# Kernel optimization log

Measured on AMD Instinct MI355X. Metric: run time of the kernel, lower is better.

## Reference

```python
import jax, jax.numpy as jnp
import numpy as np

B, S, HID = 4, 2048, 512
NH, HD = 8, 64
MAX_REL = 512


def setup_inputs() -> dict:
    key = jax.random.key(0)
    ks = jax.random.split(key, 10)
    sd = 0.02
    return {
        "hidden_states": jax.random.normal(ks[0], (B, S, HID), jnp.float32),
        "attention_mask": jnp.ones((B, S), jnp.float32),
        "Wq": jax.random.normal(ks[1], (HID, HID), jnp.float32) * sd,
        "bq": jnp.zeros((HID,), jnp.float32),
        "Wk": jax.random.normal(ks[2], (HID, HID), jnp.float32) * sd,
        "bk": jnp.zeros((HID,), jnp.float32),
        "Wv": jax.random.normal(ks[3], (HID, HID), jnp.float32) * sd,
        "bv": jnp.zeros((HID,), jnp.float32),
        "Wo": jax.random.normal(ks[4], (HID, HID), jnp.float32) * sd,
        "bo": jnp.zeros((HID,), jnp.float32),
        "rel_table": jax.random.normal(ks[5], (2 * MAX_REL + 1, NH), jnp.float32) * sd,
    }


def _heads(x):
    # [B,S,HID] -> [B,NH,S,HD]
    return x.reshape(B, S, NH, HD).transpose(0, 2, 1, 3)


def reference(hidden_states, attention_mask, Wq, bq, Wk, bk, Wv, bv, Wo, bo, rel_table):
    q = _heads(hidden_states @ Wq + bq)
    k = _heads(hidden_states @ Wk + bk)
    v = _heads(hidden_states @ Wv + bv)

    scores = jnp.einsum("bhqd,bhkd->bhqk", q, k) / jnp.sqrt(jnp.float32(HD))

    # relative position bias: rel[i,j] = clip(j-i, -MAX_REL, MAX_REL) + MAX_REL
    pos = jnp.arange(S)
    rel = jnp.clip(pos[None, :] - pos[:, None], -MAX_REL, MAX_REL) + MAX_REL
    bias = rel_table[rel]                      # [S,S,NH]
    bias = bias.transpose(2, 0, 1)             # [NH,S,S]
    scores = scores + bias[None]

    # mask: 1 attend, 0 masked
    neg = jnp.finfo(scores.dtype).min
    scores = scores + (1.0 - attention_mask)[:, None, None, :] * neg

    probs = jax.nn.softmax(scores, axis=-1)
    ctx = jnp.einsum("bhqk,bhkd->bhqd", probs, v)
    ctx = ctx.transpose(0, 2, 1, 3).reshape(B, S, HID)
    return ctx @ Wo + bo
```

## Files before the change

### kernel.cpp

```cpp
#include <hip/hip_runtime.h>
#include <hip/hip_bf16.h>

#define B_    4
#define S_    2048
#define HID_  512
#define NH_   8
#define HD_   64
#define MAXREL 512
#define M_    (B_ * S_)

#define LOG2E 1.44269504f
#define SCALE_Q (0.125f * LOG2E)

typedef __attribute__((ext_vector_type(8))) short bf8;
typedef __attribute__((ext_vector_type(4))) float f4;

static __device__ __forceinline__ unsigned short f2bf(float f) {
    union { float f; unsigned int u; } v; v.f = f;
    unsigned int u = v.u;
    unsigned int r = (u + 0x7FFFu + ((u >> 16) & 1u)) >> 16;
    return (unsigned short)r;
}

static __device__ __forceinline__ float ex2(float x) {
    float r; asm("v_exp_f32 %0, %1" : "=v"(r) : "v"(x)); return r;
}

static __device__ __forceinline__ void gload16(const void* g, void* l) {
    __builtin_amdgcn_global_load_lds(
        (const __attribute__((address_space(1))) unsigned int*)g,
        (__attribute__((address_space(3))) unsigned int*)l, 16, 0, 0);
}

#define MFMA16(a, b, c) __builtin_amdgcn_mfma_f32_16x16x32_bf16((a), (b), (c), 0, 0, 0)

__global__ void k_cast_hs(const float* __restrict__ src, unsigned short* __restrict__ dst, int n4) {
    int i = blockIdx.x * blockDim.x + threadIdx.x;
    if (i >= n4) return;
    float4 v = ((const float4*)src)[i];
    ushort4 o;
    o.x = f2bf(v.x); o.y = f2bf(v.y); o.z = f2bf(v.z); o.w = f2bf(v.w);
    ((ushort4*)dst)[i] = o;
}

__global__ void k_prep_mask(const float* __restrict__ mask, float* __restrict__ maskadd) {
    int i = blockIdx.x * blockDim.x + threadIdx.x;
    if (i < M_) maskadd[i] = (1.0f - mask[i]) * -3.0e38f;
}

__global__ void k_transpose_w4(const float* __restrict__ W0, const float* __restrict__ W1,
                               const float* __restrict__ W2, const float* __restrict__ W3,
                               unsigned short* __restrict__ T0, unsigned short* __restrict__ T1,
                               unsigned short* __restrict__ T2, unsigned short* __restrict__ T3) {
    __shared__ float tile[32][33];
    const int z = blockIdx.z;
    const float* W = (z == 0) ? W0 : (z == 1) ? W1 : (z == 2) ? W2 : W3;
    unsigned short* T = (z == 0) ? T0 : (z == 1) ? T1 : (z == 2) ? T2 : T3;
    const int tx = threadIdx.x & 31, ty = threadIdx.x >> 5;
    const int n0 = blockIdx.x * 32, k0 = blockIdx.y * 32;
    #pragma unroll
    for (int i = 0; i < 4; ++i)
        tile[ty + i * 8][tx] = W[(size_t)(k0 + ty + i * 8) * HID_ + n0 + tx];
    __syncthreads();
    #pragma unroll
    for (int i = 0; i < 4; ++i)
        T[(size_t)(n0 + ty + i * 8) * HID_ + k0 + tx] = f2bf(tile[tx][ty + i * 8]);
}

__global__ __launch_bounds__(256, 3) void k_gemm_qkv(
    const unsigned short* __restrict__ Abf,
    const unsigned short* __restrict__ Wqt, const unsigned short* __restrict__ Wkt,
    const unsigned short* __restrict__ Wvt,
    const float* __restrict__ bq, const float* __restrict__ bk, const float* __restrict__ bv,
    unsigned short* __restrict__ Q, unsigned short* __restrict__ K, unsigned short* __restrict__ Vt)
{
    __shared__ unsigned short Al[2][128 * 32];
    __shared__ unsigned short Bl[2][128 * 32];

    const int t = threadIdx.x;
    const int lane = t & 63, w = t >> 6;
    const int lr = lane & 15, lg = lane >> 4;
    const int wr = w >> 1, wc = w & 1;

    const int m0 = blockIdx.x * 128;
    const int ng = blockIdx.y * 128;
    const int z = ng >> 9;
    const int n0 = ng & 511;
    const unsigned short* Wt = (z == 0) ? Wqt : ((z == 1) ? Wkt : Wvt);
    const float* bias = (z == 0) ? bq : ((z == 1) ? bk : bv);
    const float osc = (z == 0) ? SCALE_Q : 1.0f;

    const int srow = t >> 2;
    const int sc = (((t & 3) ^ ((srow >> 1) & 3))) * 8;
    const unsigned short* Ag0 = &Abf[(size_t)(m0 + srow) * HID_ + sc];
    const unsigned short* Ag1 = &Abf[(size_t)(m0 + 64 + srow) * HID_ + sc];
    const unsigned short* Bg0 = &Wt[(size_t)(n0 + srow) * HID_ + sc];
    const unsigned short* Bg1 = &Wt[(size_t)(n0 + 64 + srow) * HID_ + sc];
    char* dA0 = (char*)&Al[0][0] + w * 1024;
    char* dB0 = (char*)&Bl[0][0] + w * 1024;

    const int fx = (lr >> 1) & 3;
    int aoff[4], boff[4];
    #pragma unroll
    for (int i = 0; i < 4; ++i) {
        aoff[i] = (wr * 64 + i * 16 + lr) * 32 + ((lg ^ fx) * 8);
        boff[i] = (wc * 64 + i * 16 + lr) * 32 + ((lg ^ fx) * 8);
    }

    gload16(Ag0, dA0);
    gload16(Ag1, dA0 + 4096);
    gload16(Bg0, dB0);
    gload16(Bg1, dB0 + 4096);
    __syncthreads();

    f4 acc[4][4] = {};
    for (int kt = 0; kt < 16; ++kt) {
        const int cur = kt & 1;
        if (kt < 15) {
            const int ko = (kt + 1) * 32;
            const int bo = (cur ^ 1) * 8192;
            gload16(Ag0 + ko, dA0 + bo);
            gload16(Ag1 + ko, dA0 + bo + 4096);
            gload16(Bg0 + ko, dB0 + bo);
            gload16(Bg1 + ko, dB0 + bo + 4096);
        }
        bf8 af[4], bf_[4];
        #pragma unroll
        for (int i = 0; i < 4; ++i) {
            af[i]  = *(const bf8*)&Al[cur][aoff[i]];
            bf_[i] = *(const bf8*)&Bl[cur][boff[i]];
        }
        #pragma unroll
        for (int mi = 0; mi < 4; ++mi)
            #pragma unroll
            for (int ni = 0; ni < 4; ++ni)
                acc[mi][ni] = MFMA16(af[mi], bf_[ni], acc[mi][ni]);
        __syncthreads();
    }

    #pragma unroll
    for (int mi = 0; mi < 4; ++mi)
    #pragma unroll
    for (int ni = 0; ni < 4; ++ni) {
        const int col = n0 + wc * 64 + ni * 16 + lr;
        const int h = col >> 6, d = col & 63;
        const float bs = bias[col];
        const int row0 = m0 + wr * 64 + mi * 16 + lg * 4;
        const int b = row0 >> 11, s0 = row0 & 2047;
        if (z == 2) {
            ushort4 o;
            o.x = f2bf(acc[mi][ni][0] + bs);
            o.y = f2bf(acc[mi][ni][1] + bs);
            o.z = f2bf(acc[mi][ni][2] + bs);
            o.w = f2bf(acc[mi][ni][3] + bs);
            *(ushort4*)&Vt[(((size_t)(b * NH_ + h)) * HD_ + d) * S_ + s0] = o;
        } else {
            unsigned short* dst = (z == 0) ? Q : K;
            #pragma unroll
            for (int r = 0; r < 4; ++r) {
                float v = (acc[mi][ni][r] + bs) * osc;
                dst[(((size_t)(b * NH_ + h)) * S_ + s0 + r) * HD_ + d] = f2bf(v);
            }
        }
    }
}

__global__ __launch_bounds__(512) void k_gemm_out(
    const unsigned short* __restrict__ Abf,
    const unsigned short* __restrict__ Wot,
    const float* __restrict__ bo,
    float* __restrict__ out)
{
    __shared__ unsigned short Al[2][128 * 32];
    __shared__ unsigned short Bl[2][128 * 32];

    const int t = threadIdx.x;
    const int lane = t & 63, w = t >> 6;
    const int lr = lane & 15, lg = lane >> 4;
    const int wr = w >> 2, wc = w & 3;

    const int m0 = blockIdx.x * 128;
    const int n0 = blockIdx.y * 128;

    const int srow = t >> 2;
    const int sc = (((t & 3) ^ ((srow >> 1) & 3))) * 8;
    const unsigned short* Ag = &Abf[(size_t)(m0 + srow) * HID_ + sc];
    const unsigned short* Bg = &Wot[(size_t)(n0 + srow) * HID_ + sc];
    char* dA = (char*)&Al[0][0] + w * 1024;
    char* dB = (char*)&Bl[0][0] + w * 1024;

    const int fx = (lr >> 1) & 3;
    int aoff[4], boff[2];
    #pragma unroll
    for (int i = 0; i < 4; ++i)
        aoff[i] = (wr * 64 + i * 16 + lr) * 32 + ((lg ^ fx) * 8);
    #pragma unroll
    for (int i = 0; i < 2; ++i)
        boff[i] = (wc * 32 + i * 16 + lr) * 32 + ((lg ^ fx) * 8);

    gload16(Ag, dA);
    gload16(Bg, dB);
    __syncthreads();

    f4 acc[4][2] = {};
    for (int kt = 0; kt < 16; ++kt) {
        const int cur = kt & 1;
        if (kt < 15) {
            const int ko = (kt + 1) * 32;
            const int bo_ = (cur ^ 1) * 8192;
            gload16(Ag + ko, dA + bo_);
            gload16(Bg + ko, dB + bo_);
        }
        bf8 af[4], bf_[2];
        #pragma unroll
        for (int i = 0; i < 4; ++i) af[i] = *(const bf8*)&Al[cur][aoff[i]];
        #pragma unroll
        for (int i = 0; i < 2; ++i) bf_[i] = *(const bf8*)&Bl[cur][boff[i]];
        #pragma unroll
        for (int mi = 0; mi < 4; ++mi)
            #pragma unroll
            for (int ni = 0; ni < 2; ++ni)
                acc[mi][ni] = MFMA16(af[mi], bf_[ni], acc[mi][ni]);
        __syncthreads();
    }

    #pragma unroll
    for (int mi = 0; mi < 4; ++mi)
    #pragma unroll
    for (int ni = 0; ni < 2; ++ni) {
        const int col = n0 + wc * 32 + ni * 16 + lr;
        const float bs = bo[col];
        const int row0 = m0 + wr * 64 + mi * 16 + lg * 4;
        #pragma unroll
        for (int r = 0; r < 4; ++r)
            out[(size_t)(row0 + r) * HID_ + col] = acc[mi][ni][r] + bs;
    }
}

__global__ __launch_bounds__(512, 4) void k_flash(
    const unsigned short* __restrict__ Q, const unsigned short* __restrict__ K,
    const unsigned short* __restrict__ Vt,
    const float* __restrict__ rel_table, const float* __restrict__ maskadd,
    unsigned short* __restrict__ ctx)
{
    __shared__ unsigned short Klds[2][4096];
    __shared__ unsigned short Vlds[2][4096];
    __shared__ unsigned short Ps[8][16][72];
    __shared__ float Tbp[2176];

    const int t = threadIdx.x;
    const int lane = t & 63, w = t >> 6;
    const int lr = lane & 15, lg = lane >> 4;

    const int flat = blockIdx.x;
    const int idx = flat >> 3;
    const int bh = (flat & 7) * 4 + (idx >> 4);
    const int qb = idx & 15;
    const int b = bh >> 3, h = bh & 7;
    const int q0 = qb * 128;

    for (int i = t; i < 2176; i += 512) {
        int r = i - q0 - 127;
        r = r < -MAXREL ? -MAXREL : (r > MAXREL ? MAXREL : r);
        Tbp[i] = rel_table[(r + MAXREL) * NH_ + h] * LOG2E;
    }
    const float TbLo = rel_table[h] * LOG2E;
    const float TbHi = rel_table[2 * MAXREL * NH_ + h] * LOG2E;

    const unsigned short* Kb = K + (size_t)bh * S_ * HD_;
    const unsigned short* Vb = Vt + (size_t)bh * HD_ * S_;
    const float* mb = maskadd + b * S_;

    const int myq = q0 + w * 16 + lr;
    const int qw = q0 + w * 16;
    bf8 qf0, qf1;
    {
        const unsigned short* qg = &Q[((size_t)bh * S_ + myq) * HD_ + lg * 8];
        qf0 = *(const bf8*)qg;
        qf1 = *(const bf8*)(qg + 32);
    }

    const int srow = w * 8 + (lane >> 3);
    const int scol = ((lane & 7) ^ (srow & 7)) * 8;
    const size_t kbase = (size_t)srow * HD_ + scol;
    const size_t vbase = (size_t)srow * S_ + scol;
    const int woff = w * 1024;

    f4 cacc[4] = {};
    float m_s = -INFINITY, lsum = 0.f;

    gload16(&Kb[kbase], (char*)&Klds[0][0] + woff);
    gload16(&Vb[vbase], (char*)&Vlds[0][0] + woff);
    __syncthreads();

    const int xr = lr & 7;
    const int jb0 = 127 - w * 16 - lr + lg * 4;
    for (int ti = 0; ti < 32; ++ti) {
        const int cur = ti & 1;
        const int kv0 = ti * 64;

        if (ti < 31) {
            const int nxt = cur ^ 1;
            gload16(&Kb[kbase + (size_t)(kv0 + 64) * HD_], (char*)&Klds[nxt][0] + woff);
            gload16(&Vb[vbase + kv0 + 64], (char*)&Vlds[nxt][0] + woff);
        }

        float4 mk[4];
        #pragma unroll
        for (int nt = 0; nt < 4; ++nt)
            mk[nt] = *(const float4*)&mb[kv0 + nt * 16 + lg * 4];

        f4 sa[4];
        #pragma unroll
        for (int nt = 0; nt < 4; ++nt) {
            const int row = (nt * 16 + lr) * 64;
            bf8 kf0 = *(const bf8*)&Klds[cur][row + ((0 + lg) ^ xr) * 8];
            bf8 kf1 = *(const bf8*)&Klds[cur][row + ((4 + lg) ^ xr) * 8];
            f4 u = {};
            u = MFMA16(kf0, qf0, u);
            u = MFMA16(kf1, qf1, u);
            sa[nt] = u;
        }

        float tmaxl = -INFINITY;
        const bool uniLo = (kv0 + 63 - qw <= -MAXREL);
        const bool uniHi = (kv0 - qw - 15 >= MAXREL);
        if (uniLo || uniHi) {
            const float biasC = uniLo ? TbLo : TbHi;
            #pragma unroll
            for (int nt = 0; nt < 4; ++nt) {
                #pragma unroll
                for (int r = 0; r < 4; ++r) {
                    float mkv = (r == 0) ? mk[nt].x : (r == 1) ? mk[nt].y : (r == 2) ? mk[nt].z : mk[nt].w;
                    float sv = sa[nt][r] + (biasC + mkv);
                    sa[nt][r] = sv;
                    tmaxl = fmaxf(tmaxl, sv);
                }
            }
        } else {
            const int jb = jb0 + kv0;
            #pragma unroll
            for (int nt = 0; nt < 4; ++nt) {
                #pragma unroll
                for (int r = 0; r < 4; ++r) {
                    float mkv = (r == 0) ? mk[nt].x : (r == 1) ? mk[nt].y : (r == 2) ? mk[nt].z : mk[nt].w;
                    float sv = sa[nt][r] + (Tbp[jb + nt * 16 + r] + mkv);
                    sa[nt][r] = sv;
                    tmaxl = fmaxf(tmaxl, sv);
                }
            }
        }
        float tmax = fmaxf(tmaxl, __shfl_xor(tmaxl, 16));
        tmax = fmaxf(tmax, __shfl_xor(tmax, 32));

        float ptile = 0.f;
        unsigned int pk[8];
        #pragma unroll
        for (int nt = 0; nt < 4; ++nt) {
            float p0 = ex2(sa[nt][0] - m_s);
            float p1 = ex2(sa[nt][1] - m_s);
            float p2 = ex2(sa[nt][2] - m_s);
            float p3 = ex2(sa[nt][3] - m_s);
            ptile += (p0 + p1) + (p2 + p3);
            asm("v_cvt_pk_bf16_f32 %0, %1, %2" : "=v"(pk[nt * 2])     : "v"(p0), "v"(p1));
            asm("v_cvt_pk_bf16_f32 %0, %1, %2" : "=v"(pk[nt * 2 + 1]) : "v"(p2), "v"(p3));
        }
        if (!__all(tmax <= m_s + 8.0f)) {
            const float mnew = fmaxf(m_s, tmax);
            const float fac = ex2(m_s - mnew);
            lsum *= fac;
            #pragma unroll
            for (int dt = 0; dt < 4; ++dt)
                #pragma unroll
                for (int r = 0; r < 4; ++r) cacc[dt][r] *= fac;
            ptile = 0.f;
            #pragma unroll
            for (int nt = 0; nt < 4; ++nt) {
                float p0 = ex2(sa[nt][0] - mnew);
                float p1 = ex2(sa[nt][1] - mnew);
                float p2 = ex2(sa[nt][2] - mnew);
                float p3 = ex2(sa[nt][3] - mnew);
                ptile += (p0 + p1) + (p2 + p3);
                asm("v_cvt_pk_bf16_f32 %0, %1, %2" : "=v"(pk[nt * 2])     : "v"(p0), "v"(p1));
                asm("v_cvt_pk_bf16_f32 %0, %1, %2" : "=v"(pk[nt * 2 + 1]) : "v"(p2), "v"(p3));
            }
            m_s = mnew;
        }
        lsum += ptile;

        #pragma unroll
        for (int nt = 0; nt < 4; ++nt) {
            uint2 pv; pv.x = pk[nt * 2]; pv.y = pk[nt * 2 + 1];
            *(uint2*)&Ps[w][lr][nt * 16 + lg * 4] = pv;
        }
        asm volatile("s_waitcnt lgkmcnt(0)" ::: "memory");
        __builtin_amdgcn_sched_barrier(0);

        #pragma unroll
        for (int kc = 0; kc < 2; ++kc) {
            bf8 pb = *(const bf8*)&Ps[w][lr][kc * 32 + lg * 8];
            #pragma unroll
            for (int dt = 0; dt < 4; ++dt) {
                const int row = (dt * 16 + lr) * 64;
                bf8 vf = *(const bf8*)&Vlds[cur][row + ((kc * 4 + lg) ^ xr) * 8];
                cacc[dt] = MFMA16(vf, pb, cacc[dt]);
            }
        }
        __syncthreads();
    }

    lsum += __shfl_xor(lsum, 16);
    lsum += __shfl_xor(lsum, 32);
    const float inv = 1.0f / lsum;
    unsigned short* cg = &ctx[(size_t)(b * S_ + myq) * HID_ + h * HD_];
    #pragma unroll
    for (int dt = 0; dt < 4; ++dt) {
        ushort4 o;
        o.x = f2bf(cacc[dt][0] * inv);
        o.y = f2bf(cacc[dt][1] * inv);
        o.z = f2bf(cacc[dt][2] * inv);
        o.w = f2bf(cacc[dt][3] * inv);
        *(ushort4*)&cg[dt * 16 + lg * 4] = o;
    }
}

extern "C" void kernel_launch(void* const* d_in, const int* in_sizes, int n_in,
                              void* d_out, int out_size, void* d_ws, size_t ws_size,
                              hipStream_t stream) {
    const float* hs  = (const float*)d_in[0];
    const float* msk = (const float*)d_in[1];
    const float* Wq  = (const float*)d_in[2];
    const float* bq  = (const float*)d_in[3];
    const float* Wk  = (const float*)d_in[4];
    const float* bk  = (const float*)d_in[5];
    const float* Wv  = (const float*)d_in[6];
    const float* bv  = (const float*)d_in[7];
    const float* Wo  = (const float*)d_in[8];
    const float* bo  = (const float*)d_in[9];
    const float* rel = (const float*)d_in[10];
    float* out = (float*)d_out;

    char* ws = (char*)d_ws;
    unsigned short* hsb = (unsigned short*)ws; ws += (size_t)M_ * HID_ * 2;
    unsigned short* Wqt = (unsigned short*)ws; ws += (size_t)HID_ * HID_ * 2;
    unsigned short* Wkt = (unsigned short*)ws; ws += (size_t)HID_ * HID_ * 2;
    unsigned short* Wvt = (unsigned short*)ws; ws += (size_t)HID_ * HID_ * 2;
    unsigned short* Wot = (unsigned short*)ws; ws += (size_t)HID_ * HID_ * 2;
    unsigned short* Qb  = (unsigned short*)ws; ws += (size_t)M_ * HID_ * 2;
    unsigned short* Kb  = (unsigned short*)ws; ws += (size_t)M_ * HID_ * 2;
    unsigned short* Vtb = (unsigned short*)ws; ws += (size_t)M_ * HID_ * 2;
    unsigned short* ctxb= (unsigned short*)ws; ws += (size_t)M_ * HID_ * 2;
    float* maskadd      = (float*)ws;          ws += (size_t)M_ * 4;

    k_cast_hs<<<(M_ * HID_ / 4 + 255) / 256, 256, 0, stream>>>(hs, hsb, M_ * HID_ / 4);
    k_prep_mask<<<(M_ + 255) / 256, 256, 0, stream>>>(msk, maskadd);
    k_transpose_w4<<<dim3(16, 16, 4), 256, 0, stream>>>(Wq, Wk, Wv, Wo, Wqt, Wkt, Wvt, Wot);
    k_gemm_qkv<<<dim3(64, 12), 256, 0, stream>>>(
        hsb, Wqt, Wkt, Wvt, bq, bk, bv, Qb, Kb, Vtb);
    k_flash<<<512, 512, 0, stream>>>(Qb, Kb, Vtb, rel, maskadd, ctxb);
    k_gemm_out<<<dim3(64, 4), 512, 0, stream>>>(ctxb, Wot, bo, out);
}
```

Baseline: 115.7 us.

## Switch flash attention to 32x32 MFMA with 4 waves of 32 query rows

The attention kernel moves from 16x16x32 to 32x32x16 bf16 MFMA tiles. The block drops from 8 waves of 16 queries to 4 waves of 32 queries, so each K/V fragment read from LDS feeds more compute, and each thread now issues two async loads per tile instead of one. It also raises wave priority around the MFMA sections and reduces the cross-lane max/sum shuffles to a single xor step. The cost is more accumulator registers per wave and fewer waves per block, which may lower latency hiding.

```diff
diff --git a/kernel.cpp b/kernel.cpp
--- a/kernel.cpp
+++ b/kernel.cpp
@@ -14,6 +14,7 @@
 
 typedef __attribute__((ext_vector_type(8))) short bf8;
 typedef __attribute__((ext_vector_type(4))) float f4;
+typedef __attribute__((ext_vector_type(16))) float f16f;
 
 static __device__ __forceinline__ unsigned short f2bf(float f) {
     union { float f; unsigned int u; } v; v.f = f;
@@ -33,6 +34,7 @@
 }
 
 #define MFMA16(a, b, c) __builtin_amdgcn_mfma_f32_16x16x32_bf16((a), (b), (c), 0, 0, 0)
+#define MFMA32(a, b, c) __builtin_amdgcn_mfma_f32_32x32x16_bf16((a), (b), (c), 0, 0, 0)
 
 __global__ void k_cast_hs(const float* __restrict__ src, unsigned short* __restrict__ dst, int n4) {
     int i = blockIdx.x * blockDim.x + threadIdx.x;
@@ -237,7 +239,7 @@
     }
 }
 
-__global__ __launch_bounds__(512, 4) void k_flash(
+__global__ __launch_bounds__(256, 2) void k_flash(
     const unsigned short* __restrict__ Q, const unsigned short* __restrict__ K,
     const unsigned short* __restrict__ Vt,
     const float* __restrict__ rel_table, const float* __restrict__ maskadd,
@@ -245,12 +247,12 @@
 {
     __shared__ unsigned short Klds[2][4096];
     __shared__ unsigned short Vlds[2][4096];
-    __shared__ unsigned short Ps[8][16][72];
+    __shared__ unsigned short Ps[4][32][68];
     __shared__ float Tbp[2176];
 
     const int t = threadIdx.x;
     const int lane = t & 63, w = t >> 6;
-    const int lr = lane & 15, lg = lane >> 4;
+    const int q = lane & 31, hi = lane >> 5;
 
     const int flat = blockIdx.x;
     const int idx = flat >> 3;
@@ -259,7 +261,7 @@
     const int b = bh >> 3, h = bh & 7;
     const int q0 = qb * 128;
 
-    for (int i = t; i < 2176; i += 512) {
+    for (int i = t; i < 2176; i += 256) {
         int r = i - q0 - 127;
         r = r < -MAXREL ? -MAXREL : (r > MAXREL ? MAXREL : r);
         Tbp[i] = rel_table[(r + MAXREL) * NH_ + h] * LOG2E;
@@ -271,156 +273,197 @@
     const unsigned short* Vb = Vt + (size_t)bh * HD_ * S_;
     const float* mb = maskadd + b * S_;
 
-    const int myq = q0 + w * 16 + lr;
-    const int qw = q0 + w * 16;
-    bf8 qf0, qf1;
-    {
-        const unsigned short* qg = &Q[((size_t)bh * S_ + myq) * HD_ + lg * 8];
-        qf0 = *(const bf8*)qg;
-        qf1 = *(const bf8*)(qg + 32);
-    }
-
-    const int srow = w * 8 + (lane >> 3);
-    const int scol = ((lane & 7) ^ (srow & 7)) * 8;
-    const size_t kbase = (size_t)srow * HD_ + scol;
-    const size_t vbase = (size_t)srow * S_ + scol;
+    const int myq = q0 + w * 32 + q;
+    const int qw = q0 + w * 32;
+    bf8 qf[4];
+    #pragma unroll
+    for (int s = 0; s < 4; ++s)
+        qf[s] = *(const bf8*)&Q[((size_t)bh * S_ + myq) * HD_ + s * 16 + hi * 8];
+
+    const int srow = t >> 3, sslot = t & 7;
+    const int sxor = (sslot ^ (srow & 7)) * 8;
+    const size_t kb0 = (size_t)srow * HD_ + sxor;
+    const size_t kb1 = (size_t)(srow + 32) * HD_ + sxor;
+    const size_t vb0 = (size_t)srow * S_ + sxor;
+    const size_t vb1 = (size_t)(srow + 32) * S_ + sxor;
     const int woff = w * 1024;
 
-    f4 cacc[4] = {};
+    f16f ca0 = {}, ca1 = {};
     float m_s = -INFINITY, lsum = 0.f;
 
-    gload16(&Kb[kbase], (char*)&Klds[0][0] + woff);
-    gload16(&Vb[vbase], (char*)&Vlds[0][0] + woff);
+    gload16(&Kb[kb0], (char*)&Klds[0][0] + woff);
+    gload16(&Kb[kb1], (char*)&Klds[0][0] + 4096 + woff);
+    gload16(&Vb[vb0], (char*)&Vlds[0][0] + woff);
+    gload16(&Vb[vb1], (char*)&Vlds[0][0] + 4096 + woff);
     __syncthreads();
 
-    const int xr = lr & 7;
-    const int jb0 = 127 - w * 16 - lr + lg * 4;
+    const int xq = q & 7;
+    const int jb0 = 127 - w * 32 - q + 4 * hi;
     for (int ti = 0; ti < 32; ++ti) {
         const int cur = ti & 1;
         const int kv0 = ti * 64;
 
         if (ti < 31) {
             const int nxt = cur ^ 1;
-            gload16(&Kb[kbase + (size_t)(kv0 + 64) * HD_], (char*)&Klds[nxt][0] + woff);
-            gload16(&Vb[vbase + kv0 + 64], (char*)&Vlds[nxt][0] + woff);
-        }
-
-        float4 mk[4];
-        #pragma unroll
-        for (int nt = 0; nt < 4; ++nt)
-            mk[nt] = *(const float4*)&mb[kv0 + nt * 16 + lg * 4];
-
-        f4 sa[4];
-        #pragma unroll
-        for (int nt = 0; nt < 4; ++nt) {
-            const int row = (nt * 16 + lr) * 64;
-            bf8 kf0 = *(const bf8*)&Klds[cur][row + ((0 + lg) ^ xr) * 8];
-            bf8 kf1 = *(const bf8*)&Klds[cur][row + ((4 + lg) ^ xr) * 8];
-            f4 u = {};
-            u = MFMA16(kf0, qf0, u);
-            u = MFMA16(kf1, qf1, u);
-            sa[nt] = u;
-        }
+            const size_t ko = (size_t)(kv0 + 64) * HD_;
+            gload16(&Kb[kb0 + ko], (char*)&Klds[nxt][0] + woff);
+            gload16(&Kb[kb1 + ko], (char*)&Klds[nxt][0] + 4096 + woff);
+            gload16(&Vb[vb0 + kv0 + 64], (char*)&Vlds[nxt][0] + woff);
+            gload16(&Vb[vb1 + kv0 + 64], (char*)&Vlds[nxt][0] + 4096 + woff);
+        }
+
+        f16f sa0 = {}, sa1 = {};
+        __builtin_amdgcn_s_setprio(1);
+        #pragma unroll
+        for (int s = 0; s < 4; ++s) {
+            const int slot = ((2 * s + hi) ^ xq) * 8;
+            bf8 k0 = *(const bf8*)&Klds[cur][q * 64 + slot];
+            bf8 k1 = *(const bf8*)&Klds[cur][(q + 32) * 64 + slot];
+            sa0 = MFMA32(k0, qf[s], sa0);
+            sa1 = MFMA32(k1, qf[s], sa1);
+        }
+        __builtin_amdgcn_s_setprio(0);
 
         float tmaxl = -INFINITY;
-        const bool uniLo = (kv0 + 63 - qw <= -MAXREL);
-        const bool uniHi = (kv0 - qw - 15 >= MAXREL);
-        if (uniLo || uniHi) {
-            const float biasC = uniLo ? TbLo : TbHi;
-            #pragma unroll
-            for (int nt = 0; nt < 4; ++nt) {
+        {
+            const bool ulo = (kv0 + 31 - qw <= -MAXREL);
+            const bool uhi = (kv0 - (qw + 31) >= MAXREL);
+            if (ulo || uhi) {
+                const float bc = ulo ? TbLo : TbHi;
                 #pragma unroll
-                for (int r = 0; r < 4; ++r) {
-                    float mkv = (r == 0) ? mk[nt].x : (r == 1) ? mk[nt].y : (r == 2) ? mk[nt].z : mk[nt].w;
-                    float sv = sa[nt][r] + (biasC + mkv);
-                    sa[nt][r] = sv;
-                    tmaxl = fmaxf(tmaxl, sv);
+                for (int m = 0; m < 4; ++m) {
+                    float4 mk = *(const float4*)&mb[kv0 + m * 8 + hi * 4];
+                    #pragma unroll
+                    for (int r = 0; r < 4; ++r) {
+                        float mkv = (r == 0) ? mk.x : (r == 1) ? mk.y : (r == 2) ? mk.z : mk.w;
+                        float sv = sa0[4 * m + r] + bc + mkv;
+                        sa0[4 * m + r] = sv;
+                        tmaxl = fmaxf(tmaxl, sv);
+                    }
+                }
+            } else {
+                #pragma unroll
+                for (int m = 0; m < 4; ++m) {
+                    float4 mk = *(const float4*)&mb[kv0 + m * 8 + hi * 4];
+                    #pragma unroll
+                    for (int r = 0; r < 4; ++r) {
+                        float mkv = (r == 0) ? mk.x : (r == 1) ? mk.y : (r == 2) ? mk.z : mk.w;
+                        float sv = sa0[4 * m + r] + Tbp[jb0 + kv0 + m * 8 + r] + mkv;
+                        sa0[4 * m + r] = sv;
+                        tmaxl = fmaxf(tmaxl, sv);
+                    }
                 }
             }
-        } else {
-            const int jb = jb0 + kv0;
-            #pragma unroll
-            for (int nt = 0; nt < 4; ++nt) {
+            const int kvh = kv0 + 32;
+            const bool ulo1 = (kvh + 31 - qw <= -MAXREL);
+            const bool uhi1 = (kvh - (qw + 31) >= MAXREL);
+            if (ulo1 || uhi1) {
+                const float bc = ulo1 ? TbLo : TbHi;
                 #pragma unroll
-                for (int r = 0; r < 4; ++r) {
-                    float mkv = (r == 0) ? mk[nt].x : (r == 1) ? mk[nt].y : (r == 2) ? mk[nt].z : mk[nt].w;
-                    float sv = sa[nt][r] + (Tbp[jb + nt * 16 + r] + mkv);
-                    sa[nt][r] = sv;
-                    tmaxl = fmaxf(tmaxl, sv);
+                for (int m = 0; m < 4; ++m) {
+                    float4 mk = *(const float4*)&mb[kvh + m * 8 + hi * 4];
+                    #pragma unroll
+                    for (int r = 0; r < 4; ++r) {
+                        float mkv = (r == 0) ? mk.x : (r == 1) ? mk.y : (r == 2) ? mk.z : mk.w;
+                        float sv = sa1[4 * m + r] + bc + mkv;
+                        sa1[4 * m + r] = sv;
+                        tmaxl = fmaxf(tmaxl, sv);
+                    }
+                }
+            } else {
+                #pragma unroll
+                for (int m = 0; m < 4; ++m) {
+                    float4 mk = *(const float4*)&mb[kvh + m * 8 + hi * 4];
+                    #pragma unroll
+                    for (int r = 0; r < 4; ++r) {
+                        float mkv = (r == 0) ? mk.x : (r == 1) ? mk.y : (r == 2) ? mk.z : mk.w;
+                        float sv = sa1[4 * m + r] + Tbp[jb0 + kvh + m * 8 + r] + mkv;
+                        sa1[4 * m + r] = sv;
+                        tmaxl = fmaxf(tmaxl, sv);
+                    }
                 }
             }
         }
-        float tmax = fmaxf(tmaxl, __shfl_xor(tmaxl, 16));
-        tmax = fmaxf(tmax, __shfl_xor(tmax, 32));
+        const float tmax = fmaxf(tmaxl, __shfl_xor(tmaxl, 32));
 
         float ptile = 0.f;
-        unsigned int pk[8];
-        #pragma unroll
-        for (int nt = 0; nt < 4; ++nt) {
-            float p0 = ex2(sa[nt][0] - m_s);
-            float p1 = ex2(sa[nt][1] - m_s);
-            float p2 = ex2(sa[nt][2] - m_s);
-            float p3 = ex2(sa[nt][3] - m_s);
-            ptile += (p0 + p1) + (p2 + p3);
-            asm("v_cvt_pk_bf16_f32 %0, %1, %2" : "=v"(pk[nt * 2])     : "v"(p0), "v"(p1));
-            asm("v_cvt_pk_bf16_f32 %0, %1, %2" : "=v"(pk[nt * 2 + 1]) : "v"(p2), "v"(p3));
+        unsigned int pkA[8], pkB[8];
+        #pragma unroll
+        for (int m = 0; m < 4; ++m) {
+            float a0 = ex2(sa0[4 * m + 0] - m_s), a1 = ex2(sa0[4 * m + 1] - m_s);
+            float a2 = ex2(sa0[4 * m + 2] - m_s), a3 = ex2(sa0[4 * m + 3] - m_s);
+            float b0 = ex2(sa1[4 * m + 0] - m_s), b1 = ex2(sa1[4 * m + 1] - m_s);
+            float b2 = ex2(sa1[4 * m + 2] - m_s), b3 = ex2(sa1[4 * m + 3] - m_s);
+            ptile += ((a0 + a1) + (a2 + a3)) + ((b0 + b1) + (b2 + b3));
+            asm("v_cvt_pk_bf16_f32 %0, %1, %2" : "=v"(pkA[2 * m])     : "v"(a0), "v"(a1));
+            asm("v_cvt_pk_bf16_f32 %0, %1, %2" : "=v"(pkA[2 * m + 1]) : "v"(a2), "v"(a3));
+            asm("v_cvt_pk_bf16_f32 %0, %1, %2" : "=v"(pkB[2 * m])     : "v"(b0), "v"(b1));
+            asm("v_cvt_pk_bf16_f32 %0, %1, %2" : "=v"(pkB[2 * m + 1]) : "v"(b2), "v"(b3));
         }
         if (!__all(tmax <= m_s + 8.0f)) {
             const float mnew = fmaxf(m_s, tmax);
             const float fac = ex2(m_s - mnew);
             lsum *= fac;
-            #pragma unroll
-            for (int dt = 0; dt < 4; ++dt)
-                #pragma unroll
-                for (int r = 0; r < 4; ++r) cacc[dt][r] *= fac;
+            ca0 *= fac;
+            ca1 *= fac;
             ptile = 0.f;
             #pragma unroll
-            for (int nt = 0; nt < 4; ++nt) {
-                float p0 = ex2(sa[nt][0] - mnew);
-                float p1 = ex2(sa[nt][1] - mnew);
-                float p2 = ex2(sa[nt][2] - mnew);
-                float p3 = ex2(sa[nt][3] - mnew);
-                ptile += (p0 + p1) + (p2 + p3);
-                asm("v_cvt_pk_bf16_f32 %0, %1, %2" : "=v"(pk[nt * 2])     : "v"(p0), "v"(p1));
-                asm("v_cvt_pk_bf16_f32 %0, %1, %2" : "=v"(pk[nt * 2 + 1]) : "v"(p2), "v"(p3));
+            for (int m = 0; m < 4; ++m) {
+                float a0 = ex2(sa0[4 * m + 0] - mnew), a1 = ex2(sa0[4 * m + 1] - mnew);
+                float a2 = ex2(sa0[4 * m + 2] - mnew), a3 = ex2(sa0[4 * m + 3] - mnew);
+                float b0 = ex2(sa1[4 * m + 0] - mnew), b1 = ex2(sa1[4 * m + 1] - mnew);
+                float b2 = ex2(sa1[4 * m + 2] - mnew), b3 = ex2(sa1[4 * m + 3] - mnew);
+                ptile += ((a0 + a1) + (a2 + a3)) + ((b0 + b1) + (b2 + b3));
+                asm("v_cvt_pk_bf16_f32 %0, %1, %2" : "=v"(pkA[2 * m])     : "v"(a0), "v"(a1));
+                asm("v_cvt_pk_bf16_f32 %0, %1, %2" : "=v"(pkA[2 * m + 1]) : "v"(a2), "v"(a3));
+                asm("v_cvt_pk_bf16_f32 %0, %1, %2" : "=v"(pkB[2 * m])     : "v"(b0), "v"(b1));
+                asm("v_cvt_pk_bf16_f32 %0, %1, %2" : "=v"(pkB[2 * m + 1]) : "v"(b2), "v"(b3));
             }
             m_s = mnew;
         }
         lsum += ptile;
 
         #pragma unroll
-        for (int nt = 0; nt < 4; ++nt) {
-            uint2 pv; pv.x = pk[nt * 2]; pv.y = pk[nt * 2 + 1];
-            *(uint2*)&Ps[w][lr][nt * 16 + lg * 4] = pv;
+        for (int m = 0; m < 4; ++m) {
+            uint2 pa; pa.x = pkA[2 * m]; pa.y = pkA[2 * m + 1];
+            *(uint2*)&Ps[w][q][m * 8 + hi * 4] = pa;
+            uint2 pb; pb.x = pkB[2 * m]; pb.y = pkB[2 * m + 1];
+            *(uint2*)&Ps[w][q][32 + m * 8 + hi * 4] = pb;
         }
         asm volatile("s_waitcnt lgkmcnt(0)" ::: "memory");
         __builtin_amdgcn_sched_barrier(0);
 
-        #pragma unroll
-        for (int kc = 0; kc < 2; ++kc) {
-            bf8 pb = *(const bf8*)&Ps[w][lr][kc * 32 + lg * 8];
-            #pragma unroll
-            for (int dt = 0; dt < 4; ++dt) {
-                const int row = (dt * 16 + lr) * 64;
-                bf8 vf = *(const bf8*)&Vlds[cur][row + ((kc * 4 + lg) ^ xr) * 8];
-                cacc[dt] = MFMA16(vf, pb, cacc[dt]);
-            }
-        }
+        __builtin_amdgcn_s_setprio(1);
+        #pragma unroll
+        for (int s = 0; s < 4; ++s) {
+            bf8 pf = *(const bf8*)&Ps[w][q][s * 16 + hi * 8];
+            const int slot = ((2 * s + hi) ^ xq) * 8;
+            bf8 v0 = *(const bf8*)&Vlds[cur][q * 64 + slot];
+            bf8 v1 = *(const bf8*)&Vlds[cur][(q + 32) * 64 + slot];
+            ca0 = MFMA32(v0, pf, ca0);
+            ca1 = MFMA32(v1, pf, ca1);
+        }
+        __builtin_amdgcn_s_setprio(0);
         __syncthreads();
     }
 
-    lsum += __shfl_xor(lsum, 16);
     lsum += __shfl_xor(lsum, 32);
     const float inv = 1.0f / lsum;
     unsigned short* cg = &ctx[(size_t)(b * S_ + myq) * HID_ + h * HD_];
     #pragma unroll
-    for (int dt = 0; dt < 4; ++dt) {
-        ushort4 o;
-        o.x = f2bf(cacc[dt][0] * inv);
-        o.y = f2bf(cacc[dt][1] * inv);
-        o.z = f2bf(cacc[dt][2] * inv);
-        o.w = f2bf(cacc[dt][3] * inv);
-        *(ushort4*)&cg[dt * 16 + lg * 4] = o;
+    for (int m = 0; m < 4; ++m) {
+        ushort4 o0;
+        o0.x = f2bf(ca0[4 * m + 0] * inv);
+        o0.y = f2bf(ca0[4 * m + 1] * inv);
+        o0.z = f2bf(ca0[4 * m + 2] * inv);
+        o0.w = f2bf(ca0[4 * m + 3] * inv);
+        *(ushort4*)&cg[m * 8 + hi * 4] = o0;
+        ushort4 o1;
+        o1.x = f2bf(ca1[4 * m + 0] * inv);
+        o1.y = f2bf(ca1[4 * m + 1] * inv);
+        o1.z = f2bf(ca1[4 * m + 2] * inv);
+        o1.w = f2bf(ca1[4 * m + 3] * inv);
+        *(ushort4*)&cg[32 + m * 8 + hi * 4] = o1;
     }
 }
 
@@ -457,6 +500,6 @@
     k_transpose_w4<<<dim3(16, 16, 4), 256, 0, stream>>>(Wq, Wk, Wv, Wo, Wqt, Wkt, Wvt, Wot);
     k_gemm_qkv<<<dim3(64, 12), 256, 0, stream>>>(
         hsb, Wqt, Wkt, Wvt, bq, bk, bv, Qb, Kb, Vtb);
-    k_flash<<<512, 512, 0, stream>>>(Qb, Kb, Vtb, rel, maskadd, ctxb);
+    k_flash<<<512, 256, 0, stream>>>(Qb, Kb, Vtb, rel, maskadd, ctxb);
     k_gemm_out<<<dim3(64, 4), 512, 0, stream>>>(ctxb, Wot, bo, out);
 }
```

Measured after the change: 119.8 us. 3.6% more time.
